# Performance work log

Hardware: AMD Instinct MI355X
Metric: run time of the kernel (lower is better)

## Reference

```python
import jax, jax.numpy as jnp
import numpy as np

B = 2; S, H, W = 14, 28, 28; C = 128; NH = 8; WS = 7; SH = 3
N = WS ** 3            # 343 tokens per window
HID = 4 * C            # 512 MLP hidden
EPS = 1e-5
SCALE = (C // NH) ** -0.5


def _rel_index():
    # reproduces the torch code exactly (meshgrid indexing='xy', quirky strides)
    coords = np.stack(np.meshgrid(np.arange(WS), np.arange(WS), np.arange(WS), indexing='xy'))  # (3,7,7,7)
    flat = coords.reshape(3, -1)                              # (3, N)
    rel = flat[:, :, None] - flat[:, None, :]                 # (3, N, N)
    rel = rel.transpose(1, 2, 0).astype(np.int64)             # (N, N, 3)
    rel[..., 0] += WS - 1
    rel[..., 1] += WS - 1
    rel[..., 2] += WS - 1
    rel[..., 0] *= 3 * WS - 1
    rel[..., 1] *= 2 * WS - 1
    return rel.sum(-1)                                        # (N, N)


def _attn_mask():
    # standard shifted-window mask: 0 where same region, -100 otherwise
    img = np.zeros((S, H, W), np.float32)
    sl = (slice(0, -WS), slice(-WS, -SH), slice(-SH, None))
    cnt = 0
    for a in sl:
        for b in sl:
            for c in sl:
                img[a, b, c] = cnt
                cnt += 1
    mw = img.reshape(S // WS, WS, H // WS, WS, W // WS, WS)
    mw = mw.transpose(0, 2, 4, 1, 3, 5).reshape(-1, N)        # (nW, N)
    am = mw[:, None, :] - mw[:, :, None]
    return jnp.asarray(np.where(am != 0, -100.0, 0.0).astype(np.float32))


def setup_inputs() -> dict:
    key = jax.random.key(0)
    ks = jax.random.split(key, 8)
    rn = lambda k, shp, s=0.02: jax.random.normal(k, shp, jnp.float32) * s
    return {
        'x': jax.random.normal(ks[0], (B, S * H * W, C), jnp.float32),
        'mask_matrix': _attn_mask(),
        'g1': jnp.ones((C,), jnp.float32), 'b1': jnp.zeros((C,), jnp.float32),
        'qkv_w': rn(ks[1], (C, 3 * C)), 'qkv_b': jnp.zeros((3 * C,), jnp.float32),
        'rpb': rn(ks[2], ((2 * WS - 1) ** 3, NH)),
        'proj_w': rn(ks[3], (C, C)), 'proj_b': jnp.zeros((C,), jnp.float32),
        'g2': jnp.ones((C,), jnp.float32), 'b2': jnp.zeros((C,), jnp.float32),
        'fc1_w': rn(ks[4], (C, HID)), 'fc1_b': jnp.zeros((HID,), jnp.float32),
        'fc2_w': rn(ks[5], (HID, C)), 'fc2_b': jnp.zeros((C,), jnp.float32),
        'rel_index': jnp.asarray(_rel_index(), jnp.int32),
    }


def _ln(x, g, b):
    mu = x.mean(-1, keepdims=True)
    d = x - mu
    var = (d * d).mean(-1, keepdims=True)
    return d * jax.lax.rsqrt(var + EPS) * g + b


def reference(x, mask_matrix, g1, b1, qkv_w, qkv_b, rpb, proj_w, proj_b,
              g2, b2, fc1_w, fc1_b, fc2_w, fc2_b, rel_index):
    shortcut = x
    h = _ln(x, g1, b1).reshape(B, S, H, W, C)
    h = jnp.roll(h, (-SH, -SH, -SH), axis=(1, 2, 3))
    # window partition -> (B_, N, C)
    h = h.reshape(B, S // WS, WS, H // WS, WS, W // WS, WS, C)
    h = h.transpose(0, 1, 3, 5, 2, 4, 6, 7).reshape(-1, N, C)
    B_ = h.shape[0]
    qkv = (h @ qkv_w + qkv_b).reshape(B_, N, 3, NH, C // NH).transpose(2, 0, 3, 1, 4)
    q, k, v = qkv[0] * SCALE, qkv[1], qkv[2]
    attn = jnp.einsum('bhnd,bhmd->bhnm', q, k)                # (B_, NH, N, N)
    bias = rpb[rel_index.reshape(-1)].reshape(N, N, NH).transpose(2, 0, 1)
    attn = attn + bias[None]
    nW = mask_matrix.shape[0]
    attn = attn.reshape(B_ // nW, nW, NH, N, N) + mask_matrix[None, :, None]
    attn = jax.nn.softmax(attn.reshape(B_, NH, N, N), axis=-1)
    o = jnp.einsum('bhnm,bhmd->bnhd', attn, v).reshape(B_, N, C)
    o = o @ proj_w + proj_b
    # window reverse -> (B, S, H, W, C)
    o = o.reshape(B, S // WS, H // WS, W // WS, WS, WS, WS, C)
    o = o.transpose(0, 1, 4, 2, 5, 3, 6, 7).reshape(B, S, H, W, C)
    o = jnp.roll(o, (SH, SH, SH), axis=(1, 2, 3)).reshape(B, S * H * W, C)
    x = shortcut + o
    y = _ln(x, g2, b2)
    y = jax.nn.gelu(y @ fc1_w + fc1_b, approximate=False) @ fc2_w + fc2_b
    return x + y
```

## Files before the change

### kernel.cpp

```cpp
#include <hip/hip_runtime.h>
#include <hip/hip_bf16.h>
#include <math.h>

typedef _Float16 half2_t __attribute__((ext_vector_type(2)));
typedef _Float16 half4_t __attribute__((ext_vector_type(4)));
typedef _Float16 half8_t __attribute__((ext_vector_type(8)));
typedef float float4_t __attribute__((ext_vector_type(4)));

#define MFMA16(a,b,c) __builtin_amdgcn_mfma_f32_16x16x16f16((a),(b),(c),0,0,0)
#define MFMA32(a,b,c) __builtin_amdgcn_mfma_f32_16x16x32_f16((a),(b),(c),0,0,0)

static __device__ __forceinline__ half2_t cvt_pk(float a, float b) {
  return __builtin_bit_cast(half2_t, __builtin_amdgcn_cvt_pkrtz(a, b));
}

static constexpr int NTOK = 21952;
static constexpr int NREG = 5488;
static constexpr float LOG2E = 1.44269504088896340736f;

__device__ __forceinline__ int rid_of(int cls, int n) {
  int z = n / 49, r = n - z*49, y = r / 7, x = r - y*7;
  int rs = (cls & 4) ? (z < 4 ? 1 : 2) : 0;
  int rh = (cls & 2) ? (y < 4 ? 1 : 2) : 0;
  int rw = (cls & 1) ? (x < 4 ? 1 : 2) : 0;
  return rs*9 + rh*3 + rw;
}

__global__ __launch_bounds__(256) void k_precomp(
    const float* __restrict__ qkv_w, const float* __restrict__ proj_w,
    const float* __restrict__ fc1_w, const float* __restrict__ fc2_w,
    const float* __restrict__ rpb,
    _Float16* __restrict__ qkv_wT, _Float16* __restrict__ proj_wT,
    _Float16* __restrict__ fc1_wT, _Float16* __restrict__ fc2_wT,
    _Float16* __restrict__ biasT, unsigned* __restrict__ bmask)
{
  int i = blockIdx.x * 256 + threadIdx.x;
  if (i < 49152) { int n = i >> 7, k = i & 127; qkv_wT[i] = (_Float16)qkv_w[k*384 + n]; return; }
  i -= 49152;
  if (i < 16384) { int n = i >> 7, k = i & 127; proj_wT[i] = (_Float16)proj_w[k*128 + n]; return; }
  i -= 16384;
  if (i < 65536) { int n = i >> 7, k = i & 127; fc1_wT[i] = (_Float16)fc1_w[k*512 + n]; return; }
  i -= 65536;
  if (i < 65536) { int n = i >> 9, k = i & 511; fc2_wT[i] = (_Float16)fc2_w[k*128 + n]; return; }
  i -= 65536;
  if (i < 8*343*352) {
    int h = i / (343*352); int r = i - h*343*352; int q = r / 352; int k = r - q*352;
    _Float16 v;
    if (k >= 343) v = (_Float16)(-30000.f);
    else {
      int zq = q/49, rq_ = q - zq*49, yq = rq_/7, xq = rq_ - yq*7;
      int zk = k/49, rk_ = k - zk*49, yk = rk_/7, xk = rk_ - yk*7;
      int idx = 20*(yq - yk + 6) + 13*(zq - zk + 6) + (xq - xk + 6);
      v = (_Float16)(rpb[idx*8 + h] * LOG2E);
    }
    biasT[i] = v;
    return;
  }
  i -= 8*343*352;
  if (i < 8*343*11) {
    int cls = i / (343*11); int r = i - cls*343*11; int q = r / 11; int kt = r - q*11;
    int rq = rid_of(cls, q);
    unsigned wbits = 0u;
    for (int j = 0; j < 32; ++j) {
      int k = kt*32 + j;
      if (k < 343 && rid_of(cls, k) == rq) wbits |= (1u << j);
    }
    bmask[i] = wbits;
  }
}

__device__ __forceinline__ void qkv_store(int row, int col, float v,
    const float* __restrict__ bias, _Float16* __restrict__ outh)
{
  v += bias[col];
  int which = col >> 7;
  if (which == 0) v *= 0.25f;
  int hh = (col >> 4) & 7, d = col & 15;
  int w = row / 343, n = row - w*343;
  size_t base = (size_t)((which*64 + w)*8 + hh)*NREG;
  if (which == 2) outh[base + d*343 + n] = (_Float16)v;
  else            outh[base + n*16  + d] = (_Float16)v;
}

__global__ __launch_bounds__(384) void k_qkv(
    const float* __restrict__ x, const float* __restrict__ g1, const float* __restrict__ b1,
    const _Float16* __restrict__ qkv_wT, const float* __restrict__ qkv_b,
    _Float16* __restrict__ qkvb, int* __restrict__ ginv)
{
  __shared__ _Float16 A[32][136];
  int mt = blockIdx.x;
  int tid = threadIdx.x, wid = tid >> 6, lane = tid & 63;
  for (int r = wid; r < 32; r += 6) {
    int row = mt*32 + r;
    int w = row / 343, n = row - w*343;
    int b = w >> 5, widx = w & 31;
    int sz = widx >> 4, sy = (widx >> 2) & 3, sx = widx & 3;
    int z = n / 49, rem = n - z*49, y = rem / 7, xx = rem - y*7;
    int gs = sz*7 + z + 3;  if (gs >= 14) gs -= 14;
    int gh = sy*7 + y + 3;  if (gh >= 28) gh -= 28;
    int gw = sx*7 + xx + 3; if (gw >= 28) gw -= 28;
    int gt = b*10976 + (gs*28 + gh)*28 + gw;
    const float* xr = x + (size_t)gt*128;
    float2 v = *(const float2*)(xr + lane*2);
    float s = v.x + v.y, sq = v.x*v.x + v.y*v.y;
    #pragma unroll
    for (int o = 1; o < 64; o <<= 1) { s += __shfl_xor(s, o); sq += __shfl_xor(sq, o); }
    float mu = s * 0.0078125f;
    float rstd = rsqrtf(sq*0.0078125f - mu*mu + 1e-5f);
    int c = lane*2;
    half2_t hv = { (_Float16)((v.x-mu)*rstd*g1[c]   + b1[c]),
                   (_Float16)((v.y-mu)*rstd*g1[c+1] + b1[c+1]) };
    *(half2_t*)&A[r][c] = hv;
    if (lane == 0) ginv[gt] = row;
  }
  __syncthreads();
  int lo = lane & 15, grp = lane >> 4;
  const _Float16* bp = qkv_wT + (size_t)(wid*64 + lo)*128 + grp*8;
  float4_t a00={0,0,0,0}, a01={0,0,0,0}, a02={0,0,0,0}, a03={0,0,0,0};
  float4_t a10={0,0,0,0}, a11={0,0,0,0}, a12={0,0,0,0}, a13={0,0,0,0};
  #pragma unroll
  for (int kk = 0; kk < 128; kk += 32) {
    half8_t f0 = *(const half8_t*)&A[lo][kk + grp*8];
    half8_t f1 = *(const half8_t*)&A[16 + lo][kk + grp*8];
    half8_t b0 = *(const half8_t*)(bp + kk);
    half8_t b1 = *(const half8_t*)(bp + kk + (size_t)16*128);
    half8_t b2 = *(const half8_t*)(bp + kk + (size_t)32*128);
    half8_t b3 = *(const half8_t*)(bp + kk + (size_t)48*128);
    a00 = MFMA32(f0, b0, a00);  a01 = MFMA32(f0, b1, a01);
    a02 = MFMA32(f0, b2, a02);  a03 = MFMA32(f0, b3, a03);
    a10 = MFMA32(f1, b0, a10);  a11 = MFMA32(f1, b1, a11);
    a12 = MFMA32(f1, b2, a12);  a13 = MFMA32(f1, b3, a13);
  }
  int row0 = mt*32 + grp*4;
  int colb = wid*64 + lo;
  #pragma unroll
  for (int r = 0; r < 4; ++r) {
    qkv_store(row0+r,    colb,    a00[r], qkv_b, qkvb);
    qkv_store(row0+r,    colb+16, a01[r], qkv_b, qkvb);
    qkv_store(row0+r,    colb+32, a02[r], qkv_b, qkvb);
    qkv_store(row0+r,    colb+48, a03[r], qkv_b, qkvb);
    qkv_store(row0+16+r, colb,    a10[r], qkv_b, qkvb);
    qkv_store(row0+16+r, colb+16, a11[r], qkv_b, qkvb);
    qkv_store(row0+16+r, colb+32, a12[r], qkv_b, qkvb);
    qkv_store(row0+16+r, colb+48, a13[r], qkv_b, qkvb);
  }
}

__global__ __launch_bounds__(512) void k_attn(
    const _Float16* __restrict__ qkv, const _Float16* __restrict__ biasT,
    const unsigned* __restrict__ bmask, _Float16* __restrict__ obuf)
{
  __shared__ _Float16 Klds[352][24];
  __shared__ _Float16 VTlds[16][360];
  int bx = blockIdx.x;
  int w = bx >> 3, h = bx & 7;
  int widx = w & 31;
  int cls = ((widx >> 4) << 2) | (((widx >> 2) & 3) == 3 ? 2 : 0) | ((widx & 3) == 3 ? 1 : 0);
  int tid = threadIdx.x;
  const _Float16* qp  = qkv + (size_t)(w*8 + h) * NREG;
  const _Float16* kp  = qp + (size_t)512  * NREG;
  const _Float16* vtp = qp + (size_t)1024 * NREG;
  for (int c = tid; c < 704; c += 512) {
    int n = c >> 1, d0 = (c & 1) * 8;
    half8_t kv = {};
    if (n < 343) kv = *(const half8_t*)(kp + n*16 + d0);
    *(half8_t*)&Klds[n][d0] = kv;
  }
  for (int c = tid; c < 704; c += 512) {
    int d = c / 44, n0 = (c - d*44) * 8;
    half8_t vv = {};
    if (n0 + 8 <= 343) vv = *(const half8_t*)(vtp + d*343 + n0);
    else { for (int j = 0; j < 8; ++j) vv[j] = (n0 + j < 343) ? vtp[d*343 + n0 + j] : (_Float16)0.f; }
    *(half8_t*)&VTlds[d][n0] = vv;
  }
  __syncthreads();
  int lane = tid & 63, lo = lane & 15, grp = lane >> 4;
  int wid = tid >> 6;
  for (int qt = wid; qt < 22; qt += 8) {
    int q  = qt*16 + lo;
    int qv = q < 343 ? q : 342;
    half4_t qf = *(const half4_t*)(qp + (size_t)qv*16 + grp*4);
    const _Float16* bp  = biasT + (size_t)(h*343 + qv)*352;
    const unsigned* bmp = bmask + (size_t)(cls*343 + qv)*11;
    half4_t barr0[11], barr1[11];
    unsigned bmarr[11];
    #pragma unroll
    for (int kt = 0; kt < 11; ++kt) {
      barr0[kt] = *(const half4_t*)(bp + kt*32 + grp*4);
      barr1[kt] = *(const half4_t*)(bp + kt*32 + 16 + grp*4);
      bmarr[kt] = bmp[kt];
    }
    float lsum = 0.f;
    float4_t acc = {0.f, 0.f, 0.f, 0.f};
    #pragma unroll
    for (int kt = 0; kt < 11; ++kt) {
      int kb = kt*32;
      half4_t ka0 = *(const half4_t*)&Klds[kb + lo][grp*4];
      half4_t ka1 = *(const half4_t*)&Klds[kb + 16 + lo][grp*4];
      float4_t zero = {0.f, 0.f, 0.f, 0.f};
      float4_t s0 = MFMA16(ka0, qf, zero);
      float4_t s1 = MFMA16(ka1, qf, zero);
      unsigned bmw = bmarr[kt];
      float p[8];
      #pragma unroll
      for (int i = 0; i < 8; ++i) {
        float sv = (i < 4) ? s0[i] : s1[i-4];
        float bb = (float)((i < 4) ? barr0[kt][i] : barr1[kt][i-4]);
        float e = exp2f(fmaf(sv, LOG2E, bb));
        unsigned bit = (bmw >> ((i >> 2)*16 + grp*4 + (i & 3))) & 1u;
        p[i] = bit ? e : 0.f;
        lsum += p[i];
      }
      half2_t pk01 = cvt_pk(p[0], p[1]);
      half2_t pk23 = cvt_pk(p[2], p[3]);
      half2_t pk45 = cvt_pk(p[4], p[5]);
      half2_t pk67 = cvt_pk(p[6], p[7]);
      half4_t pb0 = __builtin_shufflevector(pk01, pk23, 0, 1, 2, 3);
      half4_t pb1 = __builtin_shufflevector(pk45, pk67, 0, 1, 2, 3);
      half4_t va0 = *(const half4_t*)&VTlds[lo][kb + grp*4];
      half4_t va1 = *(const half4_t*)&VTlds[lo][kb + 16 + grp*4];
      acc = MFMA16(va0, pb0, acc);
      acc = MFMA16(va1, pb1, acc);
    }
    lsum += __shfl_xor(lsum, 16);
    lsum += __shfl_xor(lsum, 32);
    if (q < 343) {
      float rl = 1.f / lsum;
      half4_t o4 = { (_Float16)(acc[0]*rl), (_Float16)(acc[1]*rl),
                     (_Float16)(acc[2]*rl), (_Float16)(acc[3]*rl) };
      *(half4_t*)(obuf + (size_t)(w*343 + q)*128 + h*16 + grp*4) = o4;
    }
  }
}

__global__ __launch_bounds__(512) void k_mlp(
    const _Float16* __restrict__ obuf, const _Float16* __restrict__ proj_wT,
    const float* __restrict__ proj_b, const float* __restrict__ x,
    const int* __restrict__ ginv,
    const float* __restrict__ g2, const float* __restrict__ b2,
    const _Float16* __restrict__ fc1_wT, const float* __restrict__ fc1_b,
    float* __restrict__ x2, _Float16* __restrict__ hid)
{
  __shared__ _Float16 P[32][136];
  __shared__ float    X2[32][132];
  int mt = blockIdx.x;
  int tid = threadIdx.x, wid = tid >> 6, lane = tid & 63, lo = lane & 15, grp = lane >> 4;
  for (int r = wid; r < 32; r += 8) {
    int wrow = ginv[mt*32 + r];
    half2_t v = *(const half2_t*)(obuf + (size_t)wrow*128 + lane*2);
    *(half2_t*)&P[r][lane*2] = v;
  }
  __syncthreads();
  {
    const _Float16* bp = proj_wT + (size_t)(wid*16 + lo)*128 + grp*8;
    float4_t a0={0,0,0,0}, a1={0,0,0,0};
    #pragma unroll
    for (int kk = 0; kk < 128; kk += 32) {
      half8_t f0 = *(const half8_t*)&P[lo][kk + grp*8];
      half8_t f1 = *(const half8_t*)&P[16 + lo][kk + grp*8];
      half8_t b0 = *(const half8_t*)(bp + kk);
      a0 = MFMA32(f0, b0, a0);
      a1 = MFMA32(f1, b0, a1);
    }
    int colb = wid*16 + lo;
    float bb = proj_b[colb];
    #pragma unroll
    for (int r = 0; r < 4; ++r) {
      int r0 = grp*4 + r;
      int row0 = mt*32 + r0, row1 = row0 + 16;
      float w0 = x[(size_t)row0*128 + colb] + a0[r] + bb;
      float w1 = x[(size_t)row1*128 + colb] + a1[r] + bb;
      x2[(size_t)row0*128 + colb] = w0;  X2[r0][colb]    = w0;
      x2[(size_t)row1*128 + colb] = w1;  X2[r0+16][colb] = w1;
    }
  }
  __syncthreads();
  for (int r = wid; r < 32; r += 8) {
    float2 v = { X2[r][lane*2], X2[r][lane*2 + 1] };
    float s = v.x + v.y, sq = v.x*v.x + v.y*v.y;
    #pragma unroll
    for (int o = 1; o < 64; o <<= 1) { s += __shfl_xor(s, o); sq += __shfl_xor(sq, o); }
    float mu = s * 0.0078125f;
    float rstd = rsqrtf(sq*0.0078125f - mu*mu + 1e-5f);
    int c = lane*2;
    half2_t hv = { (_Float16)((v.x-mu)*rstd*g2[c]   + b2[c]),
                   (_Float16)((v.y-mu)*rstd*g2[c+1] + b2[c+1]) };
    *(half2_t*)&P[r][c] = hv;
  }
  __syncthreads();
  {
    const _Float16* bp = fc1_wT + (size_t)(wid*64 + lo)*128 + grp*8;
    float4_t a00={0,0,0,0}, a01={0,0,0,0}, a02={0,0,0,0}, a03={0,0,0,0};
    float4_t a10={0,0,0,0}, a11={0,0,0,0}, a12={0,0,0,0}, a13={0,0,0,0};
    #pragma unroll
    for (int kk = 0; kk < 128; kk += 32) {
      half8_t f0 = *(const half8_t*)&P[lo][kk + grp*8];
      half8_t f1 = *(const half8_t*)&P[16 + lo][kk + grp*8];
      half8_t b0 = *(const half8_t*)(bp + kk);
      half8_t b1 = *(const half8_t*)(bp + kk + (size_t)16*128);
      half8_t b2 = *(const half8_t*)(bp + kk + (size_t)32*128);
      half8_t b3 = *(const half8_t*)(bp + kk + (size_t)48*128);
      a00 = MFMA32(f0, b0, a00);  a01 = MFMA32(f0, b1, a01);
      a02 = MFMA32(f0, b2, a02);  a03 = MFMA32(f0, b3, a03);
      a10 = MFMA32(f1, b0, a10);  a11 = MFMA32(f1, b1, a11);
      a12 = MFMA32(f1, b2, a12);  a13 = MFMA32(f1, b3, a13);
    }
    int row0 = mt*32 + grp*4;
    int colb = wid*64 + lo;
    #pragma unroll
    for (int r = 0; r < 4; ++r) {
      float vv[8] = { a00[r], a01[r], a02[r], a03[r], a10[r], a11[r], a12[r], a13[r] };
      #pragma unroll
      for (int j = 0; j < 8; ++j) {
        int row = row0 + (j >= 4 ? 16 : 0) + r - r;
        int col = colb + (j & 3)*16;
        float v = vv[j] + fc1_b[col];
        float g = 0.5f * v * (1.0f + erff(v * 0.70710678118654752f));
        int rr = row0 + r + (j >= 4 ? 16 : 0);
        (void)row;
        hid[(size_t)rr*512 + col] = (_Float16)g;
      }
    }
  }
}

__global__ __launch_bounds__(256) void k_fc2(
    const _Float16* __restrict__ hid, const _Float16* __restrict__ fc2_wT,
    const float* __restrict__ fc2_b, const float* __restrict__ x2,
    float* __restrict__ out)
{
  int gw = blockIdx.x*4 + (threadIdx.x >> 6);
  int nb = gw / 1372;
  int mt = gw - nb*1372;
  int lane = threadIdx.x & 63, lo = lane & 15, grp = lane >> 4;
  const _Float16* ap = hid + (size_t)(mt*16 + lo)*512 + grp*8;
  const _Float16* bp = fc2_wT + (size_t)(nb*64 + lo)*512 + grp*8;
  float4_t acc0 = {0,0,0,0}, acc1 = {0,0,0,0}, acc2 = {0,0,0,0}, acc3 = {0,0,0,0};
  for (int kk = 0; kk < 512; kk += 32) {
    half8_t a  = *(const half8_t*)(ap + kk);
    half8_t b0 = *(const half8_t*)(bp + kk);
    half8_t b1 = *(const half8_t*)(bp + kk + (size_t)16*512);
    half8_t b2 = *(const half8_t*)(bp + kk + (size_t)32*512);
    half8_t b3 = *(const half8_t*)(bp + kk + (size_t)48*512);
    acc0 = MFMA32(a, b0, acc0);
    acc1 = MFMA32(a, b1, acc1);
    acc2 = MFMA32(a, b2, acc2);
    acc3 = MFMA32(a, b3, acc3);
  }
  int rowb = mt*16 + grp*4;
  int colb = nb*64 + lo;
  #pragma unroll
  for (int r = 0; r < 4; ++r) {
    int row = rowb + r;
    out[(size_t)row*128 + colb]      = x2[(size_t)row*128 + colb]      + acc0[r] + fc2_b[colb];
    out[(size_t)row*128 + colb + 16] = x2[(size_t)row*128 + colb + 16] + acc1[r] + fc2_b[colb+16];
    out[(size_t)row*128 + colb + 32] = x2[(size_t)row*128 + colb + 32] + acc2[r] + fc2_b[colb+32];
    out[(size_t)row*128 + colb + 48] = x2[(size_t)row*128 + colb + 48] + acc3[r] + fc2_b[colb+48];
  }
}

extern "C" void kernel_launch(void* const* d_in, const int* in_sizes, int n_in,
                              void* d_out, int out_size, void* d_ws, size_t ws_size,
                              hipStream_t stream)
{
  const float* x      = (const float*)d_in[0];
  const float* g1     = (const float*)d_in[2];
  const float* b1     = (const float*)d_in[3];
  const float* qkv_w  = (const float*)d_in[4];
  const float* qkv_b  = (const float*)d_in[5];
  const float* rpb    = (const float*)d_in[6];
  const float* proj_w = (const float*)d_in[7];
  const float* proj_b = (const float*)d_in[8];
  const float* g2     = (const float*)d_in[9];
  const float* b2     = (const float*)d_in[10];
  const float* fc1_w  = (const float*)d_in[11];
  const float* fc1_b  = (const float*)d_in[12];
  const float* fc2_w  = (const float*)d_in[13];
  const float* fc2_b  = (const float*)d_in[14];
  char* ws = (char*)d_ws;
  size_t o = 0;
  auto alloc = [&](size_t bytes) { size_t r = o; o += (bytes + 255) & ~size_t(255); return r; };
  size_t oOB  = alloc((size_t)NTOK*128*2);
  size_t oX2  = alloc((size_t)NTOK*128*4);
  size_t oU   = alloc((size_t)NTOK*512*2);
  size_t oGI  = alloc((size_t)NTOK*4);
  size_t oWQ  = alloc(49152*2);
  size_t oWP  = alloc(16384*2);
  size_t oW1  = alloc(65536*2);
  size_t oW2  = alloc(65536*2);
  size_t oBT  = alloc((size_t)8*343*352*2);
  size_t oBM  = alloc((size_t)8*343*11*4);
  (void)ws_size; (void)in_sizes; (void)n_in; (void)out_size;
  _Float16* obuf   = (_Float16*)(ws + oOB);
  float*    x2     = (float*)(ws + oX2);
  _Float16* qkvb   = (_Float16*)(ws + oU);
  _Float16* hid    = (_Float16*)(ws + oU);
  int*      ginv   = (int*)(ws + oGI);
  _Float16* qkv_wT = (_Float16*)(ws + oWQ);
  _Float16* proj_wT= (_Float16*)(ws + oWP);
  _Float16* fc1_wT = (_Float16*)(ws + oW1);
  _Float16* fc2_wT = (_Float16*)(ws + oW2);
  _Float16* biasT  = (_Float16*)(ws + oBT);
  unsigned* bmask  = (unsigned*)(ws + oBM);
  float*    out    = (float*)d_out;

  k_precomp<<<4662, 256, 0, stream>>>(qkv_w, proj_w, fc1_w, fc2_w, rpb,
                                      qkv_wT, proj_wT, fc1_wT, fc2_wT, biasT, bmask);
  k_qkv<<<686, 384, 0, stream>>>(x, g1, b1, qkv_wT, qkv_b, qkvb, ginv);
  k_attn<<<512, 512, 0, stream>>>(qkvb, biasT, bmask, obuf);
  k_mlp<<<686, 512, 0, stream>>>(obuf, proj_wT, proj_b, x, ginv, g2, b2,
                                 fc1_wT, fc1_b, x2, hid);
  k_fc2<<<686, 256, 0, stream>>>(hid, fc2_wT, fc2_b, x2, out);
}
```

Measured before the change: 128.0 us.

## Fold shift-window mask into per-class bias table and scatter attention output directly

Replaces the separate relative-position bias table and bitmask with one precomputed fp16 table per (mask class, head), where masked entries are set to -30000 so the softmax no longer needs bit tests. The attention kernel also writes its output at the un-shifted global token position, which removes the ginv inverse-index array and the gather in the MLP kernel. The trade-off is a table 8x larger (about 15 MB) that is rebuilt every call, and bias reads in attention that now hit a bigger footprint. The attention output writes are also less contiguous.

```diff
diff --git a/kernel.cpp b/kernel.cpp
--- a/kernel.cpp
+++ b/kernel.cpp
@@ -29,10 +29,8 @@
 __global__ __launch_bounds__(256) void k_precomp(
     const float* __restrict__ qkv_w, const float* __restrict__ proj_w,
     const float* __restrict__ fc1_w, const float* __restrict__ fc2_w,
-    const float* __restrict__ rpb,
     _Float16* __restrict__ qkv_wT, _Float16* __restrict__ proj_wT,
-    _Float16* __restrict__ fc1_wT, _Float16* __restrict__ fc2_wT,
-    _Float16* __restrict__ biasT, unsigned* __restrict__ bmask)
+    _Float16* __restrict__ fc1_wT, _Float16* __restrict__ fc2_wT)
 {
   int i = blockIdx.x * 256 + threadIdx.x;
   if (i < 49152) { int n = i >> 7, k = i & 127; qkv_wT[i] = (_Float16)qkv_w[k*384 + n]; return; }
@@ -41,31 +39,28 @@
   i -= 16384;
   if (i < 65536) { int n = i >> 7, k = i & 127; fc1_wT[i] = (_Float16)fc1_w[k*512 + n]; return; }
   i -= 65536;
-  if (i < 65536) { int n = i >> 9, k = i & 511; fc2_wT[i] = (_Float16)fc2_w[k*128 + n]; return; }
-  i -= 65536;
-  if (i < 8*343*352) {
-    int h = i / (343*352); int r = i - h*343*352; int q = r / 352; int k = r - q*352;
-    _Float16 v;
-    if (k >= 343) v = (_Float16)(-30000.f);
-    else {
-      int zq = q/49, rq_ = q - zq*49, yq = rq_/7, xq = rq_ - yq*7;
+  if (i < 65536) { int n = i >> 9, k = i & 511; fc2_wT[i] = (_Float16)fc2_w[k*128 + n]; }
+}
+
+__global__ __launch_bounds__(256) void k_bias(
+    const float* __restrict__ rpb, _Float16* __restrict__ biasM)
+{
+  int q  = blockIdx.x;
+  int ch = blockIdx.y;
+  int cls = ch >> 3, h = ch & 7;
+  int zq = q/49, rq_ = q - zq*49, yq = rq_/7, xq = rq_ - yq*7;
+  int ridq = rid_of(cls, q);
+  _Float16* dst = biasM + ((size_t)ch*343 + q)*352;
+  for (int k = threadIdx.x; k < 352; k += 256) {
+    _Float16 v = (_Float16)(-30000.f);
+    if (k < 343) {
       int zk = k/49, rk_ = k - zk*49, yk = rk_/7, xk = rk_ - yk*7;
-      int idx = 20*(yq - yk + 6) + 13*(zq - zk + 6) + (xq - xk + 6);
-      v = (_Float16)(rpb[idx*8 + h] * LOG2E);
-    }
-    biasT[i] = v;
-    return;
-  }
-  i -= 8*343*352;
-  if (i < 8*343*11) {
-    int cls = i / (343*11); int r = i - cls*343*11; int q = r / 11; int kt = r - q*11;
-    int rq = rid_of(cls, q);
-    unsigned wbits = 0u;
-    for (int j = 0; j < 32; ++j) {
-      int k = kt*32 + j;
-      if (k < 343 && rid_of(cls, k) == rq) wbits |= (1u << j);
-    }
-    bmask[i] = wbits;
+      if (rid_of(cls, k) == ridq) {
+        int idx = 20*(yq - yk + 6) + 13*(zq - zk + 6) + (xq - xk + 6);
+        v = (_Float16)(rpb[idx*8 + h] * LOG2E);
+      }
+    }
+    dst[k] = v;
   }
 }
 
@@ -85,7 +80,7 @@
 __global__ __launch_bounds__(384) void k_qkv(
     const float* __restrict__ x, const float* __restrict__ g1, const float* __restrict__ b1,
     const _Float16* __restrict__ qkv_wT, const float* __restrict__ qkv_b,
-    _Float16* __restrict__ qkvb, int* __restrict__ ginv)
+    _Float16* __restrict__ qkvb)
 {
   __shared__ _Float16 A[32][136];
   int mt = blockIdx.x;
@@ -111,7 +106,6 @@
     half2_t hv = { (_Float16)((v.x-mu)*rstd*g1[c]   + b1[c]),
                    (_Float16)((v.y-mu)*rstd*g1[c+1] + b1[c+1]) };
     *(half2_t*)&A[r][c] = hv;
-    if (lane == 0) ginv[gt] = row;
   }
   __syncthreads();
   int lo = lane & 15, grp = lane >> 4;
@@ -147,15 +141,16 @@
 }
 
 __global__ __launch_bounds__(512) void k_attn(
-    const _Float16* __restrict__ qkv, const _Float16* __restrict__ biasT,
-    const unsigned* __restrict__ bmask, _Float16* __restrict__ obuf)
+    const _Float16* __restrict__ qkv, const _Float16* __restrict__ biasM,
+    _Float16* __restrict__ obuf)
 {
   __shared__ _Float16 Klds[352][24];
   __shared__ _Float16 VTlds[16][360];
   int bx = blockIdx.x;
   int w = bx >> 3, h = bx & 7;
-  int widx = w & 31;
-  int cls = ((widx >> 4) << 2) | (((widx >> 2) & 3) == 3 ? 2 : 0) | ((widx & 3) == 3 ? 1 : 0);
+  int b = w >> 5, widx = w & 31;
+  int sz = widx >> 4, sy = (widx >> 2) & 3, sx = widx & 3;
+  int cls = (sz << 2) | (sy == 3 ? 2 : 0) | (sx == 3 ? 1 : 0);
   int tid = threadIdx.x;
   const _Float16* qp  = qkv + (size_t)(w*8 + h) * NREG;
   const _Float16* kp  = qp + (size_t)512  * NREG;
@@ -176,19 +171,17 @@
   __syncthreads();
   int lane = tid & 63, lo = lane & 15, grp = lane >> 4;
   int wid = tid >> 6;
+  const _Float16* btab = biasM + (size_t)(cls*8 + h)*343*352;
   for (int qt = wid; qt < 22; qt += 8) {
     int q  = qt*16 + lo;
     int qv = q < 343 ? q : 342;
     half4_t qf = *(const half4_t*)(qp + (size_t)qv*16 + grp*4);
-    const _Float16* bp  = biasT + (size_t)(h*343 + qv)*352;
-    const unsigned* bmp = bmask + (size_t)(cls*343 + qv)*11;
+    const _Float16* bp = btab + (size_t)qv*352;
     half4_t barr0[11], barr1[11];
-    unsigned bmarr[11];
     #pragma unroll
     for (int kt = 0; kt < 11; ++kt) {
       barr0[kt] = *(const half4_t*)(bp + kt*32 + grp*4);
       barr1[kt] = *(const half4_t*)(bp + kt*32 + 16 + grp*4);
-      bmarr[kt] = bmp[kt];
     }
     float lsum = 0.f;
     float4_t acc = {0.f, 0.f, 0.f, 0.f};
@@ -200,16 +193,14 @@
       float4_t zero = {0.f, 0.f, 0.f, 0.f};
       float4_t s0 = MFMA16(ka0, qf, zero);
       float4_t s1 = MFMA16(ka1, qf, zero);
-      unsigned bmw = bmarr[kt];
       float p[8];
       #pragma unroll
       for (int i = 0; i < 8; ++i) {
         float sv = (i < 4) ? s0[i] : s1[i-4];
         float bb = (float)((i < 4) ? barr0[kt][i] : barr1[kt][i-4]);
         float e = exp2f(fmaf(sv, LOG2E, bb));
-        unsigned bit = (bmw >> ((i >> 2)*16 + grp*4 + (i & 3))) & 1u;
-        p[i] = bit ? e : 0.f;
-        lsum += p[i];
+        p[i] = e;
+        lsum += e;
       }
       half2_t pk01 = cvt_pk(p[0], p[1]);
       half2_t pk23 = cvt_pk(p[2], p[3]);
@@ -225,10 +216,15 @@
     lsum += __shfl_xor(lsum, 16);
     lsum += __shfl_xor(lsum, 32);
     if (q < 343) {
+      int z = q/49, rem = q - z*49, y = rem/7, xx = rem - y*7;
+      int gs = sz*7 + z + 3;  if (gs >= 14) gs -= 14;
+      int gh = sy*7 + y + 3;  if (gh >= 28) gh -= 28;
+      int gw = sx*7 + xx + 3; if (gw >= 28) gw -= 28;
+      int gt = b*10976 + (gs*28 + gh)*28 + gw;
       float rl = 1.f / lsum;
       half4_t o4 = { (_Float16)(acc[0]*rl), (_Float16)(acc[1]*rl),
                      (_Float16)(acc[2]*rl), (_Float16)(acc[3]*rl) };
-      *(half4_t*)(obuf + (size_t)(w*343 + q)*128 + h*16 + grp*4) = o4;
+      *(half4_t*)(obuf + (size_t)gt*128 + h*16 + grp*4) = o4;
     }
   }
 }
@@ -236,7 +232,6 @@
 __global__ __launch_bounds__(512) void k_mlp(
     const _Float16* __restrict__ obuf, const _Float16* __restrict__ proj_wT,
     const float* __restrict__ proj_b, const float* __restrict__ x,
-    const int* __restrict__ ginv,
     const float* __restrict__ g2, const float* __restrict__ b2,
     const _Float16* __restrict__ fc1_wT, const float* __restrict__ fc1_b,
     float* __restrict__ x2, _Float16* __restrict__ hid)
@@ -246,8 +241,8 @@
   int mt = blockIdx.x;
   int tid = threadIdx.x, wid = tid >> 6, lane = tid & 63, lo = lane & 15, grp = lane >> 4;
   for (int r = wid; r < 32; r += 8) {
-    int wrow = ginv[mt*32 + r];
-    half2_t v = *(const half2_t*)(obuf + (size_t)wrow*128 + lane*2);
+    int row = mt*32 + r;
+    half2_t v = *(const half2_t*)(obuf + (size_t)row*128 + lane*2);
     *(half2_t*)&P[r][lane*2] = v;
   }
   __syncthreads();
@@ -312,12 +307,10 @@
       float vv[8] = { a00[r], a01[r], a02[r], a03[r], a10[r], a11[r], a12[r], a13[r] };
       #pragma unroll
       for (int j = 0; j < 8; ++j) {
-        int row = row0 + (j >= 4 ? 16 : 0) + r - r;
+        int rr  = row0 + r + (j >= 4 ? 16 : 0);
         int col = colb + (j & 3)*16;
         float v = vv[j] + fc1_b[col];
         float g = 0.5f * v * (1.0f + erff(v * 0.70710678118654752f));
-        int rr = row0 + r + (j >= 4 ? 16 : 0);
-        (void)row;
         hid[(size_t)rr*512 + col] = (_Float16)g;
       }
     }
@@ -383,32 +376,29 @@
   size_t oOB  = alloc((size_t)NTOK*128*2);
   size_t oX2  = alloc((size_t)NTOK*128*4);
   size_t oU   = alloc((size_t)NTOK*512*2);
-  size_t oGI  = alloc((size_t)NTOK*4);
   size_t oWQ  = alloc(49152*2);
   size_t oWP  = alloc(16384*2);
   size_t oW1  = alloc(65536*2);
   size_t oW2  = alloc(65536*2);
-  size_t oBT  = alloc((size_t)8*343*352*2);
-  size_t oBM  = alloc((size_t)8*343*11*4);
+  size_t oBMC = alloc((size_t)64*343*352*2);
   (void)ws_size; (void)in_sizes; (void)n_in; (void)out_size;
   _Float16* obuf   = (_Float16*)(ws + oOB);
   float*    x2     = (float*)(ws + oX2);
   _Float16* qkvb   = (_Float16*)(ws + oU);
   _Float16* hid    = (_Float16*)(ws + oU);
-  int*      ginv   = (int*)(ws + oGI);
   _Float16* qkv_wT = (_Float16*)(ws + oWQ);
   _Float16* proj_wT= (_Float16*)(ws + oWP);
   _Float16* fc1_wT = (_Float16*)(ws + oW1);
   _Float16* fc2_wT = (_Float16*)(ws + oW2);
-  _Float16* biasT  = (_Float16*)(ws + oBT);
-  unsigned* bmask  = (unsigned*)(ws + oBM);
+  _Float16* biasM  = (_Float16*)(ws + oBMC);
   float*    out    = (float*)d_out;
 
-  k_precomp<<<4662, 256, 0, stream>>>(qkv_w, proj_w, fc1_w, fc2_w, rpb,
-                                      qkv_wT, proj_wT, fc1_wT, fc2_wT, biasT, bmask);
-  k_qkv<<<686, 384, 0, stream>>>(x, g1, b1, qkv_wT, qkv_b, qkvb, ginv);
-  k_attn<<<512, 512, 0, stream>>>(qkvb, biasT, bmask, obuf);
-  k_mlp<<<686, 512, 0, stream>>>(obuf, proj_wT, proj_b, x, ginv, g2, b2,
+  k_precomp<<<768, 256, 0, stream>>>(qkv_w, proj_w, fc1_w, fc2_w,
+                                     qkv_wT, proj_wT, fc1_wT, fc2_wT);
+  k_bias<<<dim3(343, 64), 256, 0, stream>>>(rpb, biasM);
+  k_qkv<<<686, 384, 0, stream>>>(x, g1, b1, qkv_wT, qkv_b, qkvb);
+  k_attn<<<512, 512, 0, stream>>>(qkvb, biasM, obuf);
+  k_mlp<<<686, 512, 0, stream>>>(obuf, proj_wT, proj_b, x, g2, b2,
                                  fc1_wT, fc1_b, x2, hid);
   k_fc2<<<686, 256, 0, stream>>>(hid, fc2_wT, fc2_b, x2, out);
 }
```

After: 137.2 us. 1.07x slower.
